# Kernel tuning notes

Measured on AMD Instinct MI355X. Metric: run time of the kernel, lower is better.

The kernel has to match this reference:

```python
import jax, jax.numpy as jnp
import numpy as np

D_MODEL = 1024
D_HIDDEN = 4096
N_EXPERTS = 8
N_TOKENS = 4096


def setup_inputs() -> dict:
    key = jax.random.key(0)
    ks = jax.random.split(key, 7)
    s = 0.02
    return {
        "x": jax.random.normal(ks[0], (N_TOKENS, D_MODEL), dtype=jnp.float32),
        "gate_w": jax.random.normal(ks[1], (N_EXPERTS, D_MODEL), dtype=jnp.float32) * s,
        "gate_b": jnp.zeros((N_EXPERTS,), dtype=jnp.float32),
        "w1": jax.random.normal(ks[2], (N_EXPERTS, D_MODEL, D_HIDDEN), dtype=jnp.float32) * s,
        "b1": jnp.zeros((N_EXPERTS, D_HIDDEN), dtype=jnp.float32),
        "w2": jax.random.normal(ks[3], (N_EXPERTS, D_HIDDEN, D_MODEL), dtype=jnp.float32) * s,
        "b2": jnp.zeros((N_EXPERTS, D_MODEL), dtype=jnp.float32),
    }


def reference(x, gate_w, gate_b, w1, b1, w2, b2):
    # gate: softmax over expert logits, hard top-1 routing (no prob weighting,
    # matching the torch module which writes the raw expert output back)
    gate_logits = x @ gate_w.T + gate_b                      # [N, E]
    gate_probs = jax.nn.softmax(gate_logits, axis=-1)
    top_expert = jnp.argmax(gate_probs, axis=-1)             # [N] int

    # dense all-expert MLP, then one-hot select (vectorized top-1 MoE)
    h = jax.nn.relu(jnp.einsum('nd,edh->neh', x, w1) + b1[None])  # [N, E, Dh]
    y = jnp.einsum('neh,ehd->ned', h, w2) + b2[None]              # [N, E, D]
    onehot = jax.nn.one_hot(top_expert, N_EXPERTS, dtype=x.dtype)  # [N, E]
    out = jnp.einsum('ned,ne->nd', y, onehot)                      # [N, D]
    return out
```

## Files before the change

kernel.cpp:

```cpp
#include <hip/hip_runtime.h>
#include <hip/hip_bf16.h>

#define NT 4096
#define DM 1024
#define DH 4096
#define NE 8

#define BM 128
#define BN 128
#define BK 32
#define MAXT 40
#define MAXROWS 5120
#define KSPL2 2
#define BKP 40
#define G1B (8 * 4 * MAXT)

typedef short bf16x8 __attribute__((ext_vector_type(8)));
typedef float f32x4 __attribute__((ext_vector_type(4)));
typedef float f4 __attribute__((ext_vector_type(4)));

#define MI_COUNTS 0
#define MI_POFF   16
#define MI_NTILES 32
#define MI_TILEE  48
#define MI_TILER  112
#define MI_TILES0 176

#define O_BUCKET 1024ull
#define O_XB  (O_BUCKET + (size_t)NE * NT * 4)
#define O_H   (O_XB + (size_t)NT * DM * 2)
#define O_W1T (O_H + (size_t)MAXROWS * DH * 2)
#define O_W2T (O_W1T + (size_t)NE * DM * DH * 2)
#define WS_NEED (O_W2T + (size_t)NE * DH * DM * 2)
#define O_P   O_W1T

static __device__ __forceinline__ unsigned short f2bf(float f) {
  union { __hip_bfloat16 h; unsigned short u; } cv;
  cv.h = __float2bfloat16(f);
  return cv.u;
}

static __device__ __forceinline__ void gload16(const void* g, void* l) {
  __builtin_amdgcn_global_load_lds(
      (const __attribute__((address_space(1))) void*)g,
      (__attribute__((address_space(3))) void*)l, 16, 0, 0);
}

static __device__ __forceinline__ void convert_v4(
    const float* __restrict__ S, __hip_bfloat16* __restrict__ D, int N,
    int KTcnt, int kglob0, int nglob0, char* smem) {
  auto Ls = reinterpret_cast<__hip_bfloat16(*)[72]>(smem);
  const int tid = threadIdx.x;
  const int c4 = tid & 15, rk = tid >> 4;
  const float* src = S + (size_t)(kglob0 + rk * 4) * N + nglob0 + c4 * 4;
  f4 v[4];
#pragma unroll
  for (int j = 0; j < 4; ++j) v[j] = *(const f4*)(src + (size_t)j * N);
#pragma unroll
  for (int i = 0; i < 4; ++i) {
    ushort4 w;
    w.x = f2bf(v[0][i]); w.y = f2bf(v[1][i]);
    w.z = f2bf(v[2][i]); w.w = f2bf(v[3][i]);
    *(ushort4*)&Ls[c4 * 4 + i][rk * 4] = w;
  }
  __syncthreads();
  const int r = tid >> 2, q = tid & 3;
  const int nt = nglob0 >> 7;
  const int npr = (nglob0 & 64) + r;
#pragma unroll
  for (int u = 0; u < 2; ++u) {
    const int g = q * 2 + u;
    const int kt = (kglob0 >> 5) + (g >> 2);
    uint4 w = *(const uint4*)&Ls[r][g * 8];
    *(uint4*)(D + ((size_t)nt * KTcnt + kt) * 4096 + npr * 32 + (g & 3) * 8) =
        w;
  }
}

static __device__ __forceinline__ void gate_body(
    const float* __restrict__ x, const float* __restrict__ gw,
    const float* __restrict__ gb, int* __restrict__ counts,
    int* __restrict__ bucket, __hip_bfloat16* __restrict__ xb, int bid) {
  const int tid = threadIdx.x;
  const int wid = tid >> 6;
  const int lane = tid & 63;
  const int t = bid * 4 + wid;

  const f4* xrow = (const f4*)(x + (size_t)t * DM);
  ushort4* xbrow = (ushort4*)(xb + (size_t)t * DM);

  double part[NE];
#pragma unroll
  for (int e = 0; e < NE; ++e) part[e] = 0.0;

#pragma unroll
  for (int q = 0; q < 4; ++q) {
    f4 v = xrow[q * 64 + lane];
    ushort4 s;
    s.x = f2bf(v[0]); s.y = f2bf(v[1]); s.z = f2bf(v[2]); s.w = f2bf(v[3]);
    xbrow[q * 64 + lane] = s;
#pragma unroll
    for (int e = 0; e < NE; ++e) {
      f4 w = ((const f4*)(gw + (size_t)e * DM))[q * 64 + lane];
      part[e] += (double)v[0] * w[0] + (double)v[1] * w[1] +
                 (double)v[2] * w[2] + (double)v[3] * w[3];
    }
  }
#pragma unroll
  for (int off = 32; off; off >>= 1) {
#pragma unroll
    for (int e = 0; e < NE; ++e) part[e] += __shfl_down(part[e], off);
  }
  if (lane == 0) {
    double best = part[0] + (double)gb[0];
    int bi = 0;
#pragma unroll
    for (int e = 1; e < NE; ++e) {
      double le = part[e] + (double)gb[e];
      if (le > best) { best = le; bi = e; }
    }
    int pos = atomicAdd(&counts[bi], 1);
    bucket[bi * NT + pos] = t;
  }
}

__global__ __launch_bounds__(256) void gate_route_kernel(
    const float* __restrict__ x, const float* __restrict__ gw,
    const float* __restrict__ gb, int* __restrict__ counts,
    int* __restrict__ bucket, __hip_bfloat16* __restrict__ xb) {
  gate_body(x, gw, gb, counts, bucket, xb, blockIdx.x);
}

__global__ void prefix_kernel(int* __restrict__ meta, int* __restrict__ bucket) {
  if (threadIdx.x == 0) {
    int r = 0, nt = 0;
    for (int e = 0; e < NE; ++e) {
      meta[MI_POFF + e] = r;
      const int cnt = meta[MI_COUNTS + e];
      const int T = (cnt + BM - 1) / BM;
      for (int j = 0; j < T; ++j) {
        meta[MI_TILEE + nt] = e;
        meta[MI_TILER + nt] = r + j * BM;
        meta[MI_TILES0 + nt] = j * BM;
        ++nt;
      }
      r += T * BM;
    }
    meta[MI_POFF + NE] = r;
    meta[MI_NTILES] = nt;
  }
  __syncthreads();
  for (int e = 0; e < NE; ++e) {
    const int cnt = meta[MI_COUNTS + e];
    if (cnt == 0) continue;
    const int padTo = ((cnt + BM - 1) / BM) * BM;
    const int last = bucket[e * NT + cnt - 1];
    for (int i = cnt + threadIdx.x; i < padTo; i += blockDim.x)
      bucket[e * NT + i] = last;
  }
}

static __device__ __forceinline__ void gemm1_body_f32b(
    char* smem, int b, const __hip_bfloat16* __restrict__ A,
    const float* __restrict__ w1, const float* __restrict__ biasAll,
    const int* __restrict__ meta, const int* __restrict__ bucket,
    __hip_bfloat16* __restrict__ Hout) {
  auto As = reinterpret_cast<__hip_bfloat16(*)[BM][BK]>(smem);
  auto Bs = reinterpret_cast<__hip_bfloat16(*)[BN][BKP]>(smem + 16384);

  const int xcd = b & 7;
  const int idx = b >> 3;
  const int grp = idx / MAXT;
  const int tile = idx - grp * MAXT;
  const int ntile = xcd * 4 + grp;
  if (tile >= meta[MI_NTILES]) return;

  const int e = meta[MI_TILEE + tile];
  const int row0 = meta[MI_TILER + tile];
  const int s0 = meta[MI_TILES0 + tile];
  const int n0 = ntile * BN;

  const int tid = threadIdx.x;
  const int lane = tid & 63;
  const int wid = tid >> 6;
  const int lr = lane >> 2, lc = lane & 3;

  const __hip_bfloat16* aP0 =
      A + (size_t)bucket[e * NT + s0 + 32 * wid + lr] * DM + lc * 8;
  const __hip_bfloat16* aP1 =
      A + (size_t)bucket[e * NT + s0 + 32 * wid + 16 + lr] * DM + lc * 8;

  const int bc = tid & 31;
  const int bk0 = (tid >> 5) * 4;
  const float* Bp = w1 + (size_t)e * DM * DH + n0 + bc;

  const int wm = (wid >> 1) * 64, wn = (wid & 1) * 64;
  const int fr = lane & 15, ks = lane >> 4;

  f32x4 acc[4][4];
#pragma unroll
  for (int m = 0; m < 4; ++m)
#pragma unroll
    for (int n = 0; n < 4; ++n) acc[m][n] = (f32x4){0.f, 0.f, 0.f, 0.f};

  float rb[4][4];

#define BLOAD(kt)                                                     \
  do {                                                                \
    const float* bbase = Bp + (size_t)((kt) * BK + bk0) * DH;         \
    _Pragma("unroll") for (int i = 0; i < 4; ++i)                     \
        _Pragma("unroll") for (int j = 0; j < 4; ++j)                 \
            rb[i][j] = bbase[(size_t)i * DH + 32 * j];                \
  } while (0)

#define BWRITE(bf)                                                    \
  do {                                                                \
    _Pragma("unroll") for (int j = 0; j < 4; ++j) {                   \
      ushort4 w;                                                      \
      w.x = f2bf(rb[0][j]); w.y = f2bf(rb[1][j]);                     \
      w.z = f2bf(rb[2][j]); w.w = f2bf(rb[3][j]);                     \
      *(ushort4*)&Bs[bf][bc + 32 * j][bk0] = w;                       \
    }                                                                 \
  } while (0)

#define ASTAGE(bf, kt)                                                \
  do {                                                                \
    gload16(aP0 + (size_t)(kt) * BK, &As[bf][32 * wid][0]);           \
    gload16(aP1 + (size_t)(kt) * BK, &As[bf][32 * wid + 16][0]);      \
  } while (0)

#define COMPUTE(bf)                                                          \
  do {                                                                       \
    bf16x8 afr[4], bfr[4];                                                   \
    _Pragma("unroll") for (int m = 0; m < 4; ++m)                            \
        afr[m] = *(const bf16x8*)&As[bf][wm + m * 16 + fr][ks * 8];          \
    _Pragma("unroll") for (int n = 0; n < 4; ++n)                            \
        bfr[n] = *(const bf16x8*)&Bs[bf][wn + n * 16 + fr][ks * 8];          \
    _Pragma("unroll") for (int m = 0; m < 4; ++m)                            \
        _Pragma("unroll") for (int n = 0; n < 4; ++n)                        \
            acc[m][n] = __builtin_amdgcn_mfma_f32_16x16x32_bf16(             \
                afr[m], bfr[n], acc[m][n], 0, 0, 0);                         \
  } while (0)

  BLOAD(0);
  ASTAGE(0, 0);
  BWRITE(0);
  BLOAD(1);
  __syncthreads();

  for (int kt = 0; kt < 32; ++kt) {
    const int buf = kt & 1;
    if (kt + 1 < 32) {
      BWRITE(buf ^ 1);
      ASTAGE(buf ^ 1, kt + 1);
      if (kt + 2 < 32) BLOAD(kt + 2);
    }
    COMPUTE(buf);
    __syncthreads();
  }
#undef BLOAD
#undef BWRITE
#undef ASTAGE
#undef COMPUTE

  const float* bias = biasAll + (size_t)e * DH;
#pragma unroll
  for (int m = 0; m < 4; ++m)
#pragma unroll
    for (int r = 0; r < 4; ++r) {
      const int row = wm + m * 16 + ks * 4 + r;
      __hip_bfloat16* orow = Hout + (size_t)(row0 + row) * DH;
#pragma unroll
      for (int n = 0; n < 4; ++n) {
        const int col = n0 + wn + n * 16 + fr;
        float v = acc[m][n][r] + bias[col];
        orow[col] = __float2bfloat16(v > 0.f ? v : 0.f);
      }
    }
}

static __device__ __forceinline__ void gemm2_body(
    char* smem, int b, const __hip_bfloat16* __restrict__ A,
    const __hip_bfloat16* __restrict__ B, const int* __restrict__ meta,
    float* __restrict__ Pout0) {
  auto As = reinterpret_cast<__hip_bfloat16(*)[BM][BK]>(smem);
  auto Bs = reinterpret_cast<__hip_bfloat16(*)[BN][BK]>(smem + 16384);

  const int xcd = b & 7;
  const int idx = b >> 3;
  const int grp = idx / MAXT;
  const int tile = idx - grp * MAXT;
  const int np = xcd * 2 + grp;
  const int ntile = np >> 1;
  const int kq = np & 1;
  if (tile >= meta[MI_NTILES]) return;

  const int e = meta[MI_TILEE + tile];
  const int row0 = meta[MI_TILER + tile];
  const int n0 = ntile * BN;
  const int kbase = kq * (DH / KSPL2);
  const int KTcnt = DH / 32;
  const int ktb = kq * 64;

  const int tid = threadIdx.x;
  const int lane = tid & 63;
  const int wid = tid >> 6;
  const int lr = lane >> 2, lc = lane & 3;

  const __hip_bfloat16* aP0 =
      A + (size_t)(row0 + 32 * wid + lr) * DH + kbase + lc * 8;
  const __hip_bfloat16* aP1 =
      A + (size_t)(row0 + 32 * wid + 16 + lr) * DH + kbase + lc * 8;
  const __hip_bfloat16* bP0 =
      B + (((size_t)e * (DM / 128) + ntile) * KTcnt + ktb) * 4096 +
      wid * 1024 + lane * 8;
  const __hip_bfloat16* bP1 = bP0 + 512;

  const int wm = (wid >> 1) * 64, wn = (wid & 1) * 64;
  const int fr = lane & 15, ks = lane >> 4;

  f32x4 acc[4][4];
#pragma unroll
  for (int m = 0; m < 4; ++m)
#pragma unroll
    for (int n = 0; n < 4; ++n) acc[m][n] = (f32x4){0.f, 0.f, 0.f, 0.f};

#define STAGE(bf, kt)                                              \
  do {                                                             \
    gload16(aP0 + (size_t)(kt) * BK, &As[bf][32 * wid][0]);        \
    gload16(aP1 + (size_t)(kt) * BK, &As[bf][32 * wid + 16][0]);   \
    gload16(bP0 + (size_t)(kt) * 4096, &Bs[bf][32 * wid][0]);      \
    gload16(bP1 + (size_t)(kt) * 4096, &Bs[bf][32 * wid + 16][0]); \
  } while (0)

  STAGE(0, 0);
  __syncthreads();

  for (int kt = 0; kt < 64; ++kt) {
    const int buf = kt & 1;
    if (kt + 1 < 64) STAGE(buf ^ 1, kt + 1);
    bf16x8 afr[4], bfr[4];
#pragma unroll
    for (int m = 0; m < 4; ++m)
      afr[m] = *(const bf16x8*)&As[buf][wm + m * 16 + fr][ks * 8];
#pragma unroll
    for (int n = 0; n < 4; ++n)
      bfr[n] = *(const bf16x8*)&Bs[buf][wn + n * 16 + fr][ks * 8];
#pragma unroll
    for (int m = 0; m < 4; ++m)
#pragma unroll
      for (int n = 0; n < 4; ++n)
        acc[m][n] = __builtin_amdgcn_mfma_f32_16x16x32_bf16(afr[m], bfr[n],
                                                            acc[m][n], 0, 0, 0);
    __syncthreads();
  }
#undef STAGE

  float* Pout = Pout0 + (size_t)kq * MAXROWS * DM;
#pragma unroll
  for (int m = 0; m < 4; ++m)
#pragma unroll
    for (int r = 0; r < 4; ++r) {
      const int row = wm + m * 16 + ks * 4 + r;
      float* orow = Pout + (size_t)(row0 + row) * DM;
#pragma unroll
      for (int n = 0; n < 4; ++n) {
        const int col = n0 + wn + n * 16 + fr;
        orow[col] = acc[m][n][r];
      }
    }
}

__global__ __launch_bounds__(256, 2) void gemm1f_cw2_kernel(
    const __hip_bfloat16* __restrict__ xb, const float* __restrict__ w1,
    const float* __restrict__ b1, const int* __restrict__ meta,
    const int* __restrict__ bucket, __hip_bfloat16* __restrict__ h,
    const float* __restrict__ w2, __hip_bfloat16* __restrict__ w2t) {
  __shared__ __align__(16) char smem[36864];
  const int bid = blockIdx.x;
  if (bid < G1B) {
    gemm1_body_f32b(smem, bid, xb, w1, b1, meta, bucket, h);
    return;
  }
  const int id = bid - G1B;
  const int e = id >> 10;
  const int rem = id & 1023;
  const int kglob0 = (rem >> 4) * 64;
  const int nglob0 = (rem & 15) * 64;
  convert_v4(w2 + (size_t)e * DH * DM, w2t + (size_t)e * DH * DM, DM,
             DH / 32, kglob0, nglob0, smem);
}

__global__ __launch_bounds__(256, 2) void gemm2_kernel(
    const __hip_bfloat16* __restrict__ h, const __hip_bfloat16* __restrict__ w2t,
    const int* __restrict__ meta, float* __restrict__ P) {
  __shared__ __align__(16) char smem[32768];
  gemm2_body(smem, blockIdx.x, h, w2t, meta, P);
}

__global__ __launch_bounds__(256) void reduce_out_kernel(
    const float* __restrict__ P, const float* __restrict__ b2,
    const int* __restrict__ meta, const int* __restrict__ bucket,
    float* __restrict__ out) {
  const int gs = blockIdx.x;
  if (gs >= meta[MI_POFF + NE]) return;
  int e = 0;
#pragma unroll
  for (int i = 1; i < NE; ++i) e = (gs >= meta[MI_POFF + i]) ? i : e;
  const int i = gs - meta[MI_POFF + e];
  if (i >= meta[MI_COUNTS + e]) return;
  const int tok = bucket[e * NT + i];
  const int c = threadIdx.x * 4;
  float4 v = *(const float4*)(P + (size_t)gs * DM + c);
#pragma unroll
  for (int q = 1; q < KSPL2; ++q) {
    float4 p = *(const float4*)(P + ((size_t)q * MAXROWS + gs) * DM + c);
    v.x += p.x; v.y += p.y; v.z += p.z; v.w += p.w;
  }
  float4 b = *(const float4*)(b2 + (size_t)e * DM + c);
  v.x += b.x; v.y += b.y; v.z += b.z; v.w += b.w;
  *(float4*)(out + (size_t)tok * DM + c) = v;
}

template <bool RELU_BF16>
__global__ __launch_bounds__(256, 2) void moe_gemm_fallback(
    const __hip_bfloat16* __restrict__ Aall, int lda,
    const float* __restrict__ Ball, int K, int N,
    const float* __restrict__ biasAll, const int* __restrict__ counts,
    const int* __restrict__ bucket, void* __restrict__ Out, int ldo) {
  const int e = blockIdx.z;
  const int cnt = counts[e];
  const int m0 = blockIdx.y * BM;
  if (m0 >= cnt) return;
  const int n0 = blockIdx.x * BN;

  const float* Bp = Ball + (size_t)e * K * N;
  const float* bias = biasAll + (size_t)e * N;
  const int* buck = bucket + e * NT;

  __shared__ __align__(16) __hip_bfloat16 As[2][BM][BKP];
  __shared__ __align__(16) __hip_bfloat16 Bs[2][BN][BKP];

  const int tid = threadIdx.x;
  const int lane = tid & 63;
  const int wid = tid >> 6;
  const int wm = (wid >> 1) * 64;
  const int wn = (wid & 1) * 64;
  const int fr = lane & 15;
  const int ks = lane >> 4;

  const int ar = tid >> 1;
  const int ah = tid & 1;
  const int atok = buck[min(m0 + ar, cnt - 1)];
  const __hip_bfloat16* aptr = Aall + (size_t)atok * lda + ah * 16;

  const int bc = tid & 31;
  const int bk0 = (tid >> 5) * 4;

  f32x4 acc[4][4];
#pragma unroll
  for (int m = 0; m < 4; ++m)
#pragma unroll
    for (int n = 0; n < 4; ++n) acc[m][n] = (f32x4){0.f, 0.f, 0.f, 0.f};

  const int KTf = K / BK;
  uint4 ra0, ra1;
  float rb[4][4];

  {
    const uint4* p = (const uint4*)(aptr);
    ra0 = p[0]; ra1 = p[1];
    const float* bbase = Bp + (size_t)bk0 * N + n0 + bc;
#pragma unroll
    for (int i = 0; i < 4; ++i)
#pragma unroll
      for (int j = 0; j < 4; ++j) rb[i][j] = bbase[(size_t)i * N + 32 * j];
  }
  {
    *(uint4*)&As[0][ar][ah * 16] = ra0;
    *(uint4*)&As[0][ar][ah * 16 + 8] = ra1;
#pragma unroll
    for (int j = 0; j < 4; ++j) {
      ushort4 w;
      w.x = f2bf(rb[0][j]); w.y = f2bf(rb[1][j]);
      w.z = f2bf(rb[2][j]); w.w = f2bf(rb[3][j]);
      *(ushort4*)&Bs[0][bc + 32 * j][bk0] = w;
    }
  }
  __syncthreads();

  for (int kt = 0; kt < KTf; ++kt) {
    const int buf = kt & 1;
    if (kt + 1 < KTf) {
      const uint4* p = (const uint4*)(aptr + (size_t)(kt + 1) * BK);
      ra0 = p[0]; ra1 = p[1];
      const float* bbase = Bp + (size_t)((kt + 1) * BK + bk0) * N + n0 + bc;
#pragma unroll
      for (int i = 0; i < 4; ++i)
#pragma unroll
        for (int j = 0; j < 4; ++j) rb[i][j] = bbase[(size_t)i * N + 32 * j];
    }

    bf16x8 afr[4], bfr[4];
#pragma unroll
    for (int m = 0; m < 4; ++m)
      afr[m] = *(const bf16x8*)&As[buf][wm + m * 16 + fr][ks * 8];
#pragma unroll
    for (int n = 0; n < 4; ++n)
      bfr[n] = *(const bf16x8*)&Bs[buf][wn + n * 16 + fr][ks * 8];
#pragma unroll
    for (int m = 0; m < 4; ++m)
#pragma unroll
      for (int n = 0; n < 4; ++n)
        acc[m][n] = __builtin_amdgcn_mfma_f32_16x16x32_bf16(afr[m], bfr[n],
                                                            acc[m][n], 0, 0, 0);

    __syncthreads();
    if (kt + 1 < KTf) {
      *(uint4*)&As[buf ^ 1][ar][ah * 16] = ra0;
      *(uint4*)&As[buf ^ 1][ar][ah * 16 + 8] = ra1;
#pragma unroll
      for (int j = 0; j < 4; ++j) {
        ushort4 w;
        w.x = f2bf(rb[0][j]); w.y = f2bf(rb[1][j]);
        w.z = f2bf(rb[2][j]); w.w = f2bf(rb[3][j]);
        *(ushort4*)&Bs[buf ^ 1][bc + 32 * j][bk0] = w;
      }
      __syncthreads();
    }
  }

  float* outF = (float*)Out;
  __hip_bfloat16* outB = (__hip_bfloat16*)Out;
#pragma unroll
  for (int m = 0; m < 4; ++m) {
#pragma unroll
    for (int r = 0; r < 4; ++r) {
      const int row = wm + m * 16 + ks * 4 + r;
      const int slot = m0 + row;
      if (slot < cnt) {
        const int tok = buck[slot];
#pragma unroll
        for (int n = 0; n < 4; ++n) {
          const int col = n0 + wn + n * 16 + fr;
          float v = acc[m][n][r] + bias[col];
          if (RELU_BF16) {
            v = v > 0.f ? v : 0.f;
            outB[(size_t)tok * ldo + col] = __float2bfloat16(v);
          } else {
            outF[(size_t)tok * ldo + col] = v;
          }
        }
      }
    }
  }
}

extern "C" void kernel_launch(void* const* d_in, const int* in_sizes, int n_in,
                              void* d_out, int out_size, void* d_ws,
                              size_t ws_size, hipStream_t stream) {
  const float* x = (const float*)d_in[0];
  const float* gw = (const float*)d_in[1];
  const float* gb = (const float*)d_in[2];
  const float* w1 = (const float*)d_in[3];
  const float* b1 = (const float*)d_in[4];
  const float* w2 = (const float*)d_in[5];
  const float* b2 = (const float*)d_in[6];
  (void)in_sizes; (void)n_in; (void)out_size;

  char* ws = (char*)d_ws;
  int* meta = (int*)ws;
  int* counts = meta + MI_COUNTS;
  int* bucket = (int*)(ws + O_BUCKET);
  __hip_bfloat16* xb = (__hip_bfloat16*)(ws + O_XB);
  __hip_bfloat16* h = (__hip_bfloat16*)(ws + O_H);

  hipMemsetAsync(ws, 0, 1024, stream);

  if (ws_size >= WS_NEED) {
    __hip_bfloat16* w2t = (__hip_bfloat16*)(ws + O_W2T);
    float* P = (float*)(ws + O_P);

    gate_route_kernel<<<NT / 4, 256, 0, stream>>>(x, gw, gb, counts, bucket,
                                                  xb);
    prefix_kernel<<<1, 256, 0, stream>>>(meta, bucket);
    gemm1f_cw2_kernel<<<G1B + 8192, 256, 0, stream>>>(
        xb, w1, b1, meta, bucket, h, w2, w2t);
    gemm2_kernel<<<8 * 2 * MAXT, 256, 0, stream>>>(h, w2t, meta, P);
    reduce_out_kernel<<<MAXROWS, 256, 0, stream>>>(P, b2, meta, bucket,
                                                   (float*)d_out);
  } else {
    gate_route_kernel<<<NT / 4, 256, 0, stream>>>(x, gw, gb, counts, bucket,
                                                  xb);
    dim3 g1(DH / BN, NT / BM, NE);
    moe_gemm_fallback<true><<<g1, 256, 0, stream>>>(
        xb, DM, w1, DM, DH, b1, counts, bucket, (void*)h, DH);
    dim3 g2(DM / BN, NT / BM, NE);
    moe_gemm_fallback<false><<<g2, 256, 0, stream>>>(
        h, DH, w2, DH, DM, b2, counts, bucket, d_out, DM);
  }
}
```

Measured before the change: 252.7 us.

## Drop prefix kernel by decoding tiles from counts; triple-buffer gemm2 K loop

Removes the single-block prefix kernel launch. Each GEMM and reduce block now works out its expert, row offset and start index from the per-expert counts, and padding rows are clamped to cnt-1 instead of being filled into the bucket. The gemm2 main loop moves from a double buffer with two barriers per step to a three-stage LDS ring. It uses explicit vmcnt waits, so two tiles of loads stay in flight. This raises gemm2 LDS use to 48KB per block, which may reduce occupancy, and adds a small per-block decode loop.

```diff
diff --git a/kernel.cpp b/kernel.cpp
--- a/kernel.cpp
+++ b/kernel.cpp
@@ -19,13 +19,6 @@
 typedef float f32x4 __attribute__((ext_vector_type(4)));
 typedef float f4 __attribute__((ext_vector_type(4)));
 
-#define MI_COUNTS 0
-#define MI_POFF   16
-#define MI_NTILES 32
-#define MI_TILEE  48
-#define MI_TILER  112
-#define MI_TILES0 176
-
 #define O_BUCKET 1024ull
 #define O_XB  (O_BUCKET + (size_t)NE * NT * 4)
 #define O_H   (O_XB + (size_t)NT * DM * 2)
@@ -44,6 +37,29 @@
   __builtin_amdgcn_global_load_lds(
       (const __attribute__((address_space(1))) void*)g,
       (__attribute__((address_space(3))) void*)l, 16, 0, 0);
+}
+
+struct TileInfo { int e, row0, s0, cnt, valid; };
+static __device__ __forceinline__ TileInfo tile_decode(
+    const int* __restrict__ counts, int tile) {
+  TileInfo ti;
+  ti.valid = 0; ti.e = 0; ti.row0 = 0; ti.s0 = 0; ti.cnt = 0;
+  int acc = 0, r = 0;
+#pragma unroll
+  for (int q = 0; q < NE; ++q) {
+    const int c = counts[q];
+    const int T = (c + BM - 1) >> 7;
+    if (!ti.valid && tile < acc + T) {
+      ti.e = q;
+      ti.s0 = (tile - acc) * BM;
+      ti.row0 = r + ti.s0;
+      ti.cnt = c;
+      ti.valid = 1;
+    }
+    acc += T;
+    r += T * BM;
+  }
+  return ti;
 }
 
 static __device__ __forceinline__ void convert_v4(
@@ -131,39 +147,10 @@
   gate_body(x, gw, gb, counts, bucket, xb, blockIdx.x);
 }
 
-__global__ void prefix_kernel(int* __restrict__ meta, int* __restrict__ bucket) {
-  if (threadIdx.x == 0) {
-    int r = 0, nt = 0;
-    for (int e = 0; e < NE; ++e) {
-      meta[MI_POFF + e] = r;
-      const int cnt = meta[MI_COUNTS + e];
-      const int T = (cnt + BM - 1) / BM;
-      for (int j = 0; j < T; ++j) {
-        meta[MI_TILEE + nt] = e;
-        meta[MI_TILER + nt] = r + j * BM;
-        meta[MI_TILES0 + nt] = j * BM;
-        ++nt;
-      }
-      r += T * BM;
-    }
-    meta[MI_POFF + NE] = r;
-    meta[MI_NTILES] = nt;
-  }
-  __syncthreads();
-  for (int e = 0; e < NE; ++e) {
-    const int cnt = meta[MI_COUNTS + e];
-    if (cnt == 0) continue;
-    const int padTo = ((cnt + BM - 1) / BM) * BM;
-    const int last = bucket[e * NT + cnt - 1];
-    for (int i = cnt + threadIdx.x; i < padTo; i += blockDim.x)
-      bucket[e * NT + i] = last;
-  }
-}
-
 static __device__ __forceinline__ void gemm1_body_f32b(
     char* smem, int b, const __hip_bfloat16* __restrict__ A,
     const float* __restrict__ w1, const float* __restrict__ biasAll,
-    const int* __restrict__ meta, const int* __restrict__ bucket,
+    const int* __restrict__ counts, const int* __restrict__ bucket,
     __hip_bfloat16* __restrict__ Hout) {
   auto As = reinterpret_cast<__hip_bfloat16(*)[BM][BK]>(smem);
   auto Bs = reinterpret_cast<__hip_bfloat16(*)[BN][BKP]>(smem + 16384);
@@ -173,11 +160,9 @@
   const int grp = idx / MAXT;
   const int tile = idx - grp * MAXT;
   const int ntile = xcd * 4 + grp;
-  if (tile >= meta[MI_NTILES]) return;
-
-  const int e = meta[MI_TILEE + tile];
-  const int row0 = meta[MI_TILER + tile];
-  const int s0 = meta[MI_TILES0 + tile];
+  const TileInfo ti = tile_decode(counts, tile);
+  if (!ti.valid) return;
+  const int e = ti.e, row0 = ti.row0, s0 = ti.s0, cnt = ti.cnt;
   const int n0 = ntile * BN;
 
   const int tid = threadIdx.x;
@@ -185,10 +170,10 @@
   const int wid = tid >> 6;
   const int lr = lane >> 2, lc = lane & 3;
 
-  const __hip_bfloat16* aP0 =
-      A + (size_t)bucket[e * NT + s0 + 32 * wid + lr] * DM + lc * 8;
-  const __hip_bfloat16* aP1 =
-      A + (size_t)bucket[e * NT + s0 + 32 * wid + 16 + lr] * DM + lc * 8;
+  const int sa0 = min(s0 + 32 * wid + lr, cnt - 1);
+  const int sa1 = min(s0 + 32 * wid + 16 + lr, cnt - 1);
+  const __hip_bfloat16* aP0 = A + (size_t)bucket[e * NT + sa0] * DM + lc * 8;
+  const __hip_bfloat16* aP1 = A + (size_t)bucket[e * NT + sa1] * DM + lc * 8;
 
   const int bc = tid & 31;
   const int bk0 = (tid >> 5) * 4;
@@ -281,10 +266,10 @@
 
 static __device__ __forceinline__ void gemm2_body(
     char* smem, int b, const __hip_bfloat16* __restrict__ A,
-    const __hip_bfloat16* __restrict__ B, const int* __restrict__ meta,
+    const __hip_bfloat16* __restrict__ B, const int* __restrict__ counts,
     float* __restrict__ Pout0) {
   auto As = reinterpret_cast<__hip_bfloat16(*)[BM][BK]>(smem);
-  auto Bs = reinterpret_cast<__hip_bfloat16(*)[BN][BK]>(smem + 16384);
+  auto Bs = reinterpret_cast<__hip_bfloat16(*)[BN][BK]>(smem + 3 * 8192);
 
   const int xcd = b & 7;
   const int idx = b >> 3;
@@ -293,14 +278,14 @@
   const int np = xcd * 2 + grp;
   const int ntile = np >> 1;
   const int kq = np & 1;
-  if (tile >= meta[MI_NTILES]) return;
-
-  const int e = meta[MI_TILEE + tile];
-  const int row0 = meta[MI_TILER + tile];
+  const TileInfo ti = tile_decode(counts, tile);
+  if (!ti.valid) return;
+  const int e = ti.e, row0 = ti.row0;
   const int n0 = ntile * BN;
   const int kbase = kq * (DH / KSPL2);
   const int KTcnt = DH / 32;
   const int ktb = kq * 64;
+  const int KTM = 64;
 
   const int tid = threadIdx.x;
   const int lane = tid & 63;
@@ -333,28 +318,32 @@
     gload16(bP1 + (size_t)(kt) * 4096, &Bs[bf][32 * wid + 16][0]); \
   } while (0)
 
+#define COMPUTE(bf)                                                          \
+  do {                                                                       \
+    bf16x8 afr[4], bfr[4];                                                   \
+    _Pragma("unroll") for (int m = 0; m < 4; ++m)                            \
+        afr[m] = *(const bf16x8*)&As[bf][wm + m * 16 + fr][ks * 8];          \
+    _Pragma("unroll") for (int n = 0; n < 4; ++n)                            \
+        bfr[n] = *(const bf16x8*)&Bs[bf][wn + n * 16 + fr][ks * 8];          \
+    _Pragma("unroll") for (int m = 0; m < 4; ++m)                            \
+        _Pragma("unroll") for (int n = 0; n < 4; ++n)                        \
+            acc[m][n] = __builtin_amdgcn_mfma_f32_16x16x32_bf16(             \
+                afr[m], bfr[n], acc[m][n], 0, 0, 0);                         \
+  } while (0)
+
   STAGE(0, 0);
-  __syncthreads();
-
-  for (int kt = 0; kt < 64; ++kt) {
-    const int buf = kt & 1;
-    if (kt + 1 < 64) STAGE(buf ^ 1, kt + 1);
-    bf16x8 afr[4], bfr[4];
-#pragma unroll
-    for (int m = 0; m < 4; ++m)
-      afr[m] = *(const bf16x8*)&As[buf][wm + m * 16 + fr][ks * 8];
-#pragma unroll
-    for (int n = 0; n < 4; ++n)
-      bfr[n] = *(const bf16x8*)&Bs[buf][wn + n * 16 + fr][ks * 8];
-#pragma unroll
-    for (int m = 0; m < 4; ++m)
-#pragma unroll
-      for (int n = 0; n < 4; ++n)
-        acc[m][n] = __builtin_amdgcn_mfma_f32_16x16x32_bf16(afr[m], bfr[n],
-                                                            acc[m][n], 0, 0, 0);
-    __syncthreads();
-  }
+  STAGE(1, 1);
+  for (int kt = 0; kt < KTM - 1; ++kt) {
+    asm volatile("s_waitcnt vmcnt(4)" ::: "memory");
+    __builtin_amdgcn_s_barrier();
+    if (kt + 2 < KTM) STAGE((kt + 2) % 3, kt + 2);
+    COMPUTE(kt % 3);
+  }
+  asm volatile("s_waitcnt vmcnt(0)" ::: "memory");
+  __builtin_amdgcn_s_barrier();
+  COMPUTE((KTM - 1) % 3);
 #undef STAGE
+#undef COMPUTE
 
   float* Pout = Pout0 + (size_t)kq * MAXROWS * DM;
 #pragma unroll
@@ -373,13 +362,13 @@
 
 __global__ __launch_bounds__(256, 2) void gemm1f_cw2_kernel(
     const __hip_bfloat16* __restrict__ xb, const float* __restrict__ w1,
-    const float* __restrict__ b1, const int* __restrict__ meta,
+    const float* __restrict__ b1, const int* __restrict__ counts,
     const int* __restrict__ bucket, __hip_bfloat16* __restrict__ h,
     const float* __restrict__ w2, __hip_bfloat16* __restrict__ w2t) {
   __shared__ __align__(16) char smem[36864];
   const int bid = blockIdx.x;
   if (bid < G1B) {
-    gemm1_body_f32b(smem, bid, xb, w1, b1, meta, bucket, h);
+    gemm1_body_f32b(smem, bid, xb, w1, b1, counts, bucket, h);
     return;
   }
   const int id = bid - G1B;
@@ -393,22 +382,25 @@
 
 __global__ __launch_bounds__(256, 2) void gemm2_kernel(
     const __hip_bfloat16* __restrict__ h, const __hip_bfloat16* __restrict__ w2t,
-    const int* __restrict__ meta, float* __restrict__ P) {
-  __shared__ __align__(16) char smem[32768];
-  gemm2_body(smem, blockIdx.x, h, w2t, meta, P);
+    const int* __restrict__ counts, float* __restrict__ P) {
+  __shared__ __align__(16) char smem[49152];
+  gemm2_body(smem, blockIdx.x, h, w2t, counts, P);
 }
 
 __global__ __launch_bounds__(256) void reduce_out_kernel(
     const float* __restrict__ P, const float* __restrict__ b2,
-    const int* __restrict__ meta, const int* __restrict__ bucket,
+    const int* __restrict__ counts, const int* __restrict__ bucket,
     float* __restrict__ out) {
   const int gs = blockIdx.x;
-  if (gs >= meta[MI_POFF + NE]) return;
-  int e = 0;
-#pragma unroll
-  for (int i = 1; i < NE; ++i) e = (gs >= meta[MI_POFF + i]) ? i : e;
-  const int i = gs - meta[MI_POFF + e];
-  if (i >= meta[MI_COUNTS + e]) return;
+  int r = 0, e = -1, i = 0, cnt_e = 0;
+#pragma unroll
+  for (int q = 0; q < NE; ++q) {
+    const int c = counts[q];
+    const int pad = ((c + BM - 1) >> 7) << 7;
+    if (e < 0 && gs >= r && gs < r + pad) { e = q; i = gs - r; cnt_e = c; }
+    r += pad;
+  }
+  if (e < 0 || i >= cnt_e) return;
   const int tok = bucket[e * NT + i];
   const int c = threadIdx.x * 4;
   float4 v = *(const float4*)(P + (size_t)gs * DM + c);
@@ -569,8 +561,7 @@
   (void)in_sizes; (void)n_in; (void)out_size;
 
   char* ws = (char*)d_ws;
-  int* meta = (int*)ws;
-  int* counts = meta + MI_COUNTS;
+  int* counts = (int*)ws;
   int* bucket = (int*)(ws + O_BUCKET);
   __hip_bfloat16* xb = (__hip_bfloat16*)(ws + O_XB);
   __hip_bfloat16* h = (__hip_bfloat16*)(ws + O_H);
@@ -583,11 +574,10 @@
 
     gate_route_kernel<<<NT / 4, 256, 0, stream>>>(x, gw, gb, counts, bucket,
                                                   xb);
-    prefix_kernel<<<1, 256, 0, stream>>>(meta, bucket);
     gemm1f_cw2_kernel<<<G1B + 8192, 256, 0, stream>>>(
-        xb, w1, b1, meta, bucket, h, w2, w2t);
-    gemm2_kernel<<<8 * 2 * MAXT, 256, 0, stream>>>(h, w2t, meta, P);
-    reduce_out_kernel<<<MAXROWS, 256, 0, stream>>>(P, b2, meta, bucket,
+        xb, w1, b1, counts, bucket, h, w2, w2t);
+    gemm2_kernel<<<8 * 2 * MAXT, 256, 0, stream>>>(h, w2t, counts, P);
+    reduce_out_kernel<<<MAXROWS, 256, 0, stream>>>(P, b2, counts, bucket,
                                                    (float*)d_out);
   } else {
     gate_route_kernel<<<NT / 4, 256, 0, stream>>>(x, gw, gb, counts, bucket,
```

Measured after the change: 250.8 us. About the same (-0.7%).
